# Kernel tuning notes

Hardware: AMD Instinct MI355X
Metric: run time of the kernel (lower is better)

## Reference

```python
import jax, jax.numpy as jnp
import numpy as np

L_IN, L_ENC, B = 1024, 1024, 16
D_IN, D_ENC, D_EMB = 512, 512, 512


def setup_inputs() -> dict:
    key = jax.random.key(0)
    ks = jax.random.split(key, 9)
    s_in = 1.0 / np.sqrt(D_IN)
    s_emb = 1.0 / np.sqrt(D_EMB)
    s_enc = 1.0 / np.sqrt(D_ENC)
    return {
        "in_seq": jax.random.normal(ks[0], (L_IN, B, D_IN), jnp.float32),
        "enc_seq": jax.random.normal(ks[1], (L_ENC, B, D_ENC), jnp.float32),
        "prev_target_seq": jax.random.normal(ks[2], (L_IN, B, D_EMB), jnp.float32),
        # torch Linear weights: (out_features, in_features)
        "W_in2enc": jax.random.normal(ks[3], (D_ENC, D_IN), jnp.float32) * s_in,
        "b_in2enc": jnp.zeros((D_ENC,), jnp.float32),
        "W_lab2enc": jax.random.normal(ks[4], (D_ENC, D_EMB), jnp.float32) * s_emb,
        "b_lab2enc": jnp.zeros((D_ENC,), jnp.float32),
        "W_enc2in": jax.random.normal(ks[5], (D_IN, D_ENC), jnp.float32) * s_enc,
        "b_enc2in": jnp.zeros((D_IN,), jnp.float32),
    }


def reference(in_seq, enc_seq, prev_target_seq,
              W_in2enc, b_in2enc, W_lab2enc, b_lab2enc, W_enc2in, b_enc2in):
    # d_vals: (L_in, B, D_enc) = proj(in_seq) + proj(prev_target_seq)
    in_proj = jnp.einsum('lbi,ei->lbe', in_seq, W_in2enc) + b_in2enc
    tgt_proj = jnp.einsum('lbm,em->lbe', prev_target_seq, W_lab2enc) + b_lab2enc
    d_vals = in_proj + tgt_proj
    # raw attention scores: (L_in, L_enc, B) dot products over D_enc
    scores = jnp.einsum('lbe,mbe->lmb', d_vals, enc_seq)
    # sum-normalization (NOT softmax) over the encoder-length axis
    attn = scores / jnp.sum(scores, axis=1, keepdims=True)
    # weighted sum of encoder states: (L_in, B, D_enc)
    context = jnp.einsum('lmb,mbe->lbe', attn, enc_seq)
    # project back to input dim
    return jnp.einsum('lbe,ie->lbi', context, W_enc2in) + b_enc2in
```

## Files before the change

kernel.cpp:

```cpp
#include <hip/hip_runtime.h>
#include <cstdint>

static constexpr int LDR = 8192;

typedef uint16_t u16;
typedef __attribute__((ext_vector_type(8))) short short8;
typedef __attribute__((ext_vector_type(4))) float f32x4;
struct alignas(8) U16x4 { u16 x, y, z, w; };

__device__ __forceinline__ u16 f2bf(float f) {
    union { float f; unsigned u; } v; v.f = f;
    unsigned r = v.u + 0x7fffu + ((v.u >> 16) & 1u);
    return (u16)(r >> 16);
}

__device__ __forceinline__ short8 cvt8(const float4 a, const float4 b) {
    short8 r;
    r[0]=(short)f2bf(a.x); r[1]=(short)f2bf(a.y); r[2]=(short)f2bf(a.z); r[3]=(short)f2bf(a.w);
    r[4]=(short)f2bf(b.x); r[5]=(short)f2bf(b.y); r[6]=(short)f2bf(b.z); r[7]=(short)f2bf(b.w);
    return r;
}

__device__ __forceinline__ void gl_lds16(const u16* g, unsigned ldsaddr) {
    asm volatile("s_mov_b32 m0, %0\n\t"
                 "global_load_lds_dwordx4 %1, off"
                 :: "s"(__builtin_amdgcn_readfirstlane(ldsaddr)), "v"(g)
                 : "memory");
}

template<int MODE>
__device__ __forceinline__ void gemm_body(
    int bx, int by, int z,
    const u16* __restrict__ A, const u16* __restrict__ Bm,
    const float* __restrict__ b1v, const float* __restrict__ b2v,
    const float* __restrict__ b3v, const float* __restrict__ Sinv,
    u16* __restrict__ Cb, float* __restrict__ Cf)
{
    constexpr int K   = (MODE == 1 || MODE == 5) ? 1024 : 512;
    constexpr int BM  = (MODE == 5 || MODE == 6) ? 64 : 128;
    constexpr int NJ  = (BM == 128) ? 4 : 2;
    constexpr int NIA = BM / 32;
    constexpr int NIB = 4;
    constexpr int ASZ = BM * 128;
    constexpr int BSZ = 128 * 128;
    constexpr int LDA = (MODE == 1 || MODE == 5) ? 1024 : 512;
    constexpr int LDB = (MODE == 1 || MODE == 5) ? 1024 : 512;

    extern __shared__ __align__(16) u16 lds[];

    const int row0 = by * BM;
    const int col0 = bx * 128;
    const int tid  = threadIdx.x;
    const int l    = tid & 63, w = tid >> 6;
    const int wm   = (BM == 128) ? (w >> 1) : 0;
    const int wn   = (BM == 128) ? (w & 1) : w;
    const int quad = l >> 4, l16 = l & 15;

    const u16* Ab = A;
    const u16* Bb = Bm;
    if constexpr (MODE == 5) { Ab = A + z*524288; Bb = Bm + z*524288; }
    if constexpr (MODE == 6) { Bb = Bm + z*262144; }
    if constexpr (MODE == 4) { Ab = A + z*524288; Bb = Bm + z*262144; }

    const int lq = l >> 3;
    const int loffu = ((l & 7) ^ lq) * 8;
    const u16* gA[NIA];
    #pragma unroll
    for (int i = 0; i < NIA; ++i)
        gA[i] = Ab + (size_t)(row0 + i*32 + w*8 + lq) * LDA + loffu;
    const u16* gB[NIB];
    #pragma unroll
    for (int i = 0; i < NIB; ++i)
        gB[i] = Bb + (size_t)(col0 + i*32 + w*8 + lq) * LDB + loffu;

    const unsigned lbase = (unsigned)(size_t)&lds[0];

    auto stage = [&](int c) {
        #pragma unroll
        for (int i = 0; i < NIA; ++i) {
            gl_lds16(gA[i], lbase + c*ASZ + i*4096 + w*1024);
            gA[i] += 64;
        }
        #pragma unroll
        for (int i = 0; i < NIB; ++i) {
            gl_lds16(gB[i], lbase + 2*ASZ + c*BSZ + i*4096 + w*1024);
            gB[i] += 64;
        }
    };

    f32x4 acc[4][NJ] = {};
    const int swzr = (l16 & 7) << 3;
    const int arow = wm * 64;
    const int brow = wn * (BM == 128 ? 64 : 32);

    stage(0);
    int cur = 0;
    for (int kb = 0; kb < K; kb += 64) {
        asm volatile("s_waitcnt vmcnt(0)" ::: "memory");
        __syncthreads();
        if (kb + 64 < K) stage(cur ^ 1);
        const int abase = cur * (ASZ/2);
        const int bbase = ASZ + cur * (BSZ/2);
        #pragma unroll
        for (int kk = 0; kk < 2; ++kk) {
            const int koff = (kk*32 + quad*8) ^ swzr;
            short8 af[4], bfr[NJ];
            #pragma unroll
            for (int i = 0; i < 4; ++i)
                af[i] = *(const short8*)&lds[abase + (arow + i*16 + l16)*64 + koff];
            #pragma unroll
            for (int j = 0; j < NJ; ++j)
                bfr[j] = *(const short8*)&lds[bbase + (brow + j*16 + l16)*64 + koff];
            #pragma unroll
            for (int i = 0; i < 4; ++i)
                #pragma unroll
                for (int j = 0; j < NJ; ++j)
                    acc[i][j] = __builtin_amdgcn_mfma_f32_16x16x32_bf16(af[i], bfr[j], acc[i][j], 0, 0, 0);
        }
        cur ^= 1;
    }

    #pragma unroll
    for (int i = 0; i < 4; ++i) {
        const int grow = row0 + arow + i*16 + quad*4;
        #pragma unroll
        for (int j = 0; j < NJ; ++j) {
            const int gcol = col0 + brow + j*16 + l16;
            #pragma unroll
            for (int r = 0; r < 4; ++r) {
                float v = acc[i][j][r];
                const int R = grow + r;
                if constexpr (MODE == 1) {
                    v += b1v[gcol] + b2v[gcol];
                    Cb[((R & 15)*1024 + (R >> 4))*512 + gcol] = f2bf(v);
                } else if constexpr (MODE == 5 || MODE == 6) {
                    Cb[z*262144 + R*512 + gcol] = f2bf(v);
                } else {
                    const float s = Sinv[R*16 + z];
                    Cf[(R*16 + z)*512 + gcol] = v * s + b3v[gcol];
                }
            }
        }
    }
}

__device__ __forceinline__ void s_xt_body(
    int bid, const float* __restrict__ X, const float* __restrict__ T,
    const double* __restrict__ u, const double* __restrict__ cd,
    float* __restrict__ Sinv, u16* __restrict__ XT)
{
    const int wave = threadIdx.x >> 6, lane = threadIdx.x & 63;
    const int b = bid & 15, g = bid >> 4;
    const int e = lane * 8;
    double u1r[8], u2r[8];
    #pragma unroll
    for (int k = 0; k < 8; ++k) {
        u1r[k] = u[b*512 + e + k];
        u2r[k] = u[8192 + b*512 + e + k];
    }
    const double cb = cd[b];
    #pragma unroll 2
    for (int i = 0; i < 8; ++i) {
        const int j = g*32 + wave*8 + i;
        const int r = j*16 + b;
        float4 x0 = *(const float4*)&X[r*512 + e];
        float4 x1 = *(const float4*)&X[r*512 + e + 4];
        float4 t0 = *(const float4*)&T[r*512 + e];
        float4 t1 = *(const float4*)&T[r*512 + e + 4];
        double a = 0.0;
        a += (double)x0.x*u1r[0] + (double)x0.y*u1r[1] + (double)x0.z*u1r[2] + (double)x0.w*u1r[3];
        a += (double)x1.x*u1r[4] + (double)x1.y*u1r[5] + (double)x1.z*u1r[6] + (double)x1.w*u1r[7];
        a += (double)t0.x*u2r[0] + (double)t0.y*u2r[1] + (double)t0.z*u2r[2] + (double)t0.w*u2r[3];
        a += (double)t1.x*u2r[4] + (double)t1.y*u2r[5] + (double)t1.z*u2r[6] + (double)t1.w*u2r[7];
        *(short8*)&XT[r*1024 + e]       = cvt8(x0, x1);
        *(short8*)&XT[r*1024 + 512 + e] = cvt8(t0, t1);
        #pragma unroll
        for (int off = 32; off > 0; off >>= 1) a += __shfl_down(a, off, 64);
        if (lane == 0) Sinv[r] = (float)(1.0 / (a + cb));
    }
}

__global__ __launch_bounds__(256) void enct_wconv(
    const float* __restrict__ E, u16* __restrict__ EncT, double* __restrict__ part,
    const float* __restrict__ W1, const float* __restrict__ W2,
    const float* __restrict__ W3, u16* __restrict__ W12, u16* __restrict__ W3b)
{
    const int bid = blockIdx.x, t = threadIdx.x;
    if (bid >= 2048) {
        const int idx = (bid - 2048)*256 + t;
        if (idx < 65536) {
            const int r = idx >> 7, k8 = (idx & 127) * 8;
            const float* src = (k8 < 512) ? (W1 + r*512 + k8) : (W2 + r*512 + (k8 - 512));
            float4 a = *(const float4*)src;
            float4 b = *((const float4*)src + 1);
            *(short8*)&W12[r*1024 + k8] = cvt8(a, b);
        } else {
            const int i2 = idx - 65536;
            const int r = i2 >> 6, k8 = (i2 & 63) * 8;
            const float* src = W3 + r*512 + k8;
            float4 a = *(const float4*)src;
            float4 b = *((const float4*)src + 1);
            *(short8*)&W3b[r*512 + k8] = cvt8(a, b);
        }
        return;
    }
    __shared__ float tile[64][65];
    __shared__ double sred[256];
    const int ex = bid & 7;
    const int my = (bid >> 3) & 15;
    const int bb = bid >> 7;
    const int m0 = my * 64;
    const int e0 = ex * 64;
    const int tr = t >> 4;
    const int tc4 = (t & 15) * 4;
    #pragma unroll
    for (int it = 0; it < 4; ++it) {
        const int ml = tr + it*16;
        float4 v = *(const float4*)&E[(m0+ml)*LDR + bb*512 + e0 + tc4];
        *(float4*)&tile[ml][tc4] = v;
    }
    __syncthreads();
    #pragma unroll
    for (int it = 0; it < 4; ++it) {
        const int el = tr + it*16;
        U16x4 o;
        o.x = f2bf(tile[tc4+0][el]);
        o.y = f2bf(tile[tc4+1][el]);
        o.z = f2bf(tile[tc4+2][el]);
        o.w = f2bf(tile[tc4+3][el]);
        *(U16x4*)&EncT[bb*524288 + (e0+el)*1024 + m0 + tc4] = o;
    }
    const int el = t & 63, mq = t >> 6;
    double a = 0.0;
    #pragma unroll
    for (int j = 0; j < 16; ++j) a += (double)tile[mq*16 + j][el];
    sred[t] = a;
    __syncthreads();
    if (t < 64) {
        double s = sred[t] + sred[t+64] + sred[t+128] + sred[t+192];
        part[my*8192 + bb*512 + e0 + t] = s;
    }
}

__global__ __launch_bounds__(256) void prep80(
    const float* __restrict__ W1, const float* __restrict__ W2,
    const float* __restrict__ b1, const float* __restrict__ b2,
    const double* __restrict__ part, double* __restrict__ u, double* __restrict__ cd)
{
    const int blk = blockIdx.x, tid = threadIdx.x;
    __shared__ double es_l[512];
    __shared__ double red[256];
    int b;
    if (blk < 64) b = (blk & 31) >> 1;
    else          b = blk - 64;
    for (int e = tid; e < 512; e += 256) {
        double s = 0.0;
        #pragma unroll
        for (int c = 0; c < 16; ++c) s += part[c*8192 + b*512 + e];
        es_l[e] = s;
    }
    __syncthreads();
    if (blk < 64) {
        const int which = blk >> 5;
        const int t = (blk & 31)*256 + tid;
        const int i = t & 511;
        const float* W = which ? W2 : W1;
        double a = 0.0;
        for (int e = 0; e < 512; ++e) a += (double)W[e*512 + i] * es_l[e];
        u[which*8192 + t] = a;
    } else {
        double a = 0.0;
        for (int e = tid; e < 512; e += 256) a += (double)(b1[e] + b2[e]) * es_l[e];
        red[tid] = a; __syncthreads();
        for (int s = 128; s > 0; s >>= 1) { if (tid < s) red[tid] += red[tid+s]; __syncthreads(); }
        if (tid == 0) cd[b] = red[0];
    }
}

__global__ __launch_bounds__(256) void fused_a(
    const float* __restrict__ X, const float* __restrict__ T,
    const double* __restrict__ u, const double* __restrict__ cd,
    float* __restrict__ Sinv, u16* __restrict__ XT,
    const u16* __restrict__ EncT, u16* __restrict__ Gram)
{
    const int bid = blockIdx.x;
    if (bid < 512) {
        s_xt_body(bid, X, T, u, cd, Sinv, XT);
    } else {
        const int idx = bid - 512;
        gemm_body<5>(idx & 3, (idx >> 2) & 7, idx >> 5,
                     EncT, EncT, nullptr, nullptr, nullptr, nullptr, Gram, nullptr);
    }
}

__global__ __launch_bounds__(256) void fused_b(
    const u16* __restrict__ XT, const u16* __restrict__ W12,
    const float* __restrict__ b1, const float* __restrict__ b2,
    u16* __restrict__ dvals_g,
    const u16* __restrict__ W3b, const u16* __restrict__ Gram,
    u16* __restrict__ HT)
{
    const int bid = blockIdx.x;
    if (bid < 512) {
        gemm_body<1>(bid & 3, bid >> 2, 0,
                     XT, W12, b1, b2, nullptr, nullptr, dvals_g, nullptr);
    } else {
        const int idx = bid - 512;
        gemm_body<6>(idx & 3, (idx >> 2) & 7, idx >> 5,
                     W3b, Gram, nullptr, nullptr, nullptr, nullptr, HT, nullptr);
    }
}

__global__ __launch_bounds__(256) void gemm_m4(
    const u16* __restrict__ dvals_g, const u16* __restrict__ HT,
    const float* __restrict__ b3, const float* __restrict__ Sinv,
    float* __restrict__ out)
{
    gemm_body<4>(blockIdx.x, blockIdx.y, blockIdx.z,
                 dvals_g, HT, nullptr, nullptr, b3, Sinv, nullptr, out);
}

extern "C" void kernel_launch(void* const* d_in, const int* in_sizes, int n_in,
                              void* d_out, int out_size, void* d_ws, size_t ws_size,
                              hipStream_t stream)
{
    const float* X   = (const float*)d_in[0];
    const float* Enc = (const float*)d_in[1];
    const float* T   = (const float*)d_in[2];
    const float* W1  = (const float*)d_in[3];
    const float* b1  = (const float*)d_in[4];
    const float* W2  = (const float*)d_in[5];
    const float* b2  = (const float*)d_in[6];
    const float* W3  = (const float*)d_in[7];
    const float* b3  = (const float*)d_in[8];
    float* out = (float*)d_out;

    char* w = (char*)d_ws;
    u16*    dvals_g  = (u16*)(w);
    u16*    EncT_bf  = (u16*)(w + 16777216);
    u16*    Gram_bf  = (u16*)(w + 33554432);
    u16*    HT_bf    = (u16*)(w + 41943040);
    u16*    W12      = (u16*)(w + 50331648);
    u16*    W3b      = (u16*)(w + 51380224);
    double* part     = (double*)(w + 51904512);
    double* u        = (double*)(w + 52953088);
    double* cd       = (double*)(w + 53084160);
    float*  Sinv     = (float*)(w + 53084288);
    u16*    XTb      = (u16*)d_out;

    dim3 blk(256);
    enct_wconv <<<dim3(2432), blk, 0, stream>>>(Enc, EncT_bf, part, W1, W2, W3, W12, W3b);
    prep80     <<<dim3(80),   blk, 0, stream>>>(W1, W2, b1, b2, part, u, cd);
    fused_a    <<<dim3(1024), blk, 49152, stream>>>(X, T, u, cd, Sinv, XTb, EncT_bf, Gram_bf);
    fused_b    <<<dim3(1024), blk, 65536, stream>>>(XTb, W12, b1, b2, dvals_g, W3b, Gram_bf, HT_bf);
    gemm_m4    <<<dim3(4, 8, 16), blk, 65536, stream>>>(dvals_g, HT_bf, b3, Sinv, out);
}
```

Measured before the change: 241.6 us.

## Regroup kernel fusions across stages, remap blocks for XCD locality, raise MFMA priority

The Gram GEMM (mode 5) now runs together with the prep reduction, and the HT GEMM (mode 6) is interleaved with the S/XT conversion, so work that does not depend on each other shares a launch. The mode 1 and mode 4 GEMMs each get their own launch. Those launches use a block-index swizzle so that consecutive logical tiles land on the same XCD and share L2. Mode 5 and 6 tiles raise wave priority with s_setprio around the MFMA loop so they are favoured over the co-resident memory-bound blocks. The costs are a different dependency schedule and a prep path that reuses the dynamic LDS.

```diff
diff --git a/kernel.cpp b/kernel.cpp
--- a/kernel.cpp
+++ b/kernel.cpp
@@ -45,6 +45,7 @@
     constexpr int BSZ = 128 * 128;
     constexpr int LDA = (MODE == 1 || MODE == 5) ? 1024 : 512;
     constexpr int LDB = (MODE == 1 || MODE == 5) ? 1024 : 512;
+    constexpr bool PRIO = (MODE == 5 || MODE == 6);
 
     extern __shared__ __align__(16) u16 lds[];
 
@@ -101,6 +102,7 @@
         if (kb + 64 < K) stage(cur ^ 1);
         const int abase = cur * (ASZ/2);
         const int bbase = ASZ + cur * (BSZ/2);
+        if constexpr (PRIO) __builtin_amdgcn_s_setprio(1);
         #pragma unroll
         for (int kk = 0; kk < 2; ++kk) {
             const int koff = (kk*32 + quad*8) ^ swzr;
@@ -117,6 +119,7 @@
                 for (int j = 0; j < NJ; ++j)
                     acc[i][j] = __builtin_amdgcn_mfma_f32_16x16x32_bf16(af[i], bfr[j], acc[i][j], 0, 0, 0);
         }
+        if constexpr (PRIO) __builtin_amdgcn_s_setprio(0);
         cur ^= 1;
     }
 
@@ -242,14 +245,22 @@
     }
 }
 
-__global__ __launch_bounds__(256) void prep80(
+__global__ __launch_bounds__(256) void g5_prep(
+    const u16* __restrict__ EncT, u16* __restrict__ Gram,
     const float* __restrict__ W1, const float* __restrict__ W2,
     const float* __restrict__ b1, const float* __restrict__ b2,
     const double* __restrict__ part, double* __restrict__ u, double* __restrict__ cd)
 {
-    const int blk = blockIdx.x, tid = threadIdx.x;
-    __shared__ double es_l[512];
-    __shared__ double red[256];
+    const int bid = blockIdx.x, tid = threadIdx.x;
+    if (bid < 512) {
+        gemm_body<5>(bid & 3, (bid >> 2) & 7, bid >> 5,
+                     EncT, EncT, nullptr, nullptr, nullptr, nullptr, Gram, nullptr);
+        return;
+    }
+    extern __shared__ __align__(16) u16 lds[];
+    double* es_l = (double*)lds;
+    double* red  = (double*)((char*)lds + 4096);
+    const int blk = bid - 512;
     int b;
     if (blk < 64) b = (blk & 31) >> 1;
     else          b = blk - 64;
@@ -277,38 +288,31 @@
     }
 }
 
-__global__ __launch_bounds__(256) void fused_a(
+__global__ __launch_bounds__(256) void g6_sxt(
+    const u16* __restrict__ W3b, const u16* __restrict__ Gram, u16* __restrict__ HT,
     const float* __restrict__ X, const float* __restrict__ T,
     const double* __restrict__ u, const double* __restrict__ cd,
-    float* __restrict__ Sinv, u16* __restrict__ XT,
-    const u16* __restrict__ EncT, u16* __restrict__ Gram)
+    float* __restrict__ Sinv, u16* __restrict__ XT)
 {
     const int bid = blockIdx.x;
-    if (bid < 512) {
-        s_xt_body(bid, X, T, u, cd, Sinv, XT);
+    const int idx = bid >> 1;
+    if (bid & 1) {
+        s_xt_body(idx, X, T, u, cd, Sinv, XT);
     } else {
-        const int idx = bid - 512;
-        gemm_body<5>(idx & 3, (idx >> 2) & 7, idx >> 5,
-                     EncT, EncT, nullptr, nullptr, nullptr, nullptr, Gram, nullptr);
-    }
-}
-
-__global__ __launch_bounds__(256) void fused_b(
+        gemm_body<6>(idx & 3, (idx >> 2) & 7, idx >> 5,
+                     W3b, Gram, nullptr, nullptr, nullptr, nullptr, HT, nullptr);
+    }
+}
+
+__global__ __launch_bounds__(256) void gemm_m1(
     const u16* __restrict__ XT, const u16* __restrict__ W12,
     const float* __restrict__ b1, const float* __restrict__ b2,
-    u16* __restrict__ dvals_g,
-    const u16* __restrict__ W3b, const u16* __restrict__ Gram,
-    u16* __restrict__ HT)
+    u16* __restrict__ dvals_g)
 {
     const int bid = blockIdx.x;
-    if (bid < 512) {
-        gemm_body<1>(bid & 3, bid >> 2, 0,
-                     XT, W12, b1, b2, nullptr, nullptr, dvals_g, nullptr);
-    } else {
-        const int idx = bid - 512;
-        gemm_body<6>(idx & 3, (idx >> 2) & 7, idx >> 5,
-                     W3b, Gram, nullptr, nullptr, nullptr, nullptr, HT, nullptr);
-    }
+    const int logical = (bid & 7)*64 + (bid >> 3);
+    gemm_body<1>(logical & 3, logical >> 2, 0,
+                 XT, W12, b1, b2, nullptr, nullptr, dvals_g, nullptr);
 }
 
 __global__ __launch_bounds__(256) void gemm_m4(
@@ -316,7 +320,9 @@
     const float* __restrict__ b3, const float* __restrict__ Sinv,
     float* __restrict__ out)
 {
-    gemm_body<4>(blockIdx.x, blockIdx.y, blockIdx.z,
+    const int bid = blockIdx.x;
+    const int logical = (bid & 7)*64 + (bid >> 3);
+    gemm_body<4>(logical & 3, (logical >> 2) & 7, logical >> 5,
                  dvals_g, HT, nullptr, nullptr, b3, Sinv, nullptr, out);
 }
 
@@ -349,9 +355,9 @@
     u16*    XTb      = (u16*)d_out;
 
     dim3 blk(256);
-    enct_wconv <<<dim3(2432), blk, 0, stream>>>(Enc, EncT_bf, part, W1, W2, W3, W12, W3b);
-    prep80     <<<dim3(80),   blk, 0, stream>>>(W1, W2, b1, b2, part, u, cd);
-    fused_a    <<<dim3(1024), blk, 49152, stream>>>(X, T, u, cd, Sinv, XTb, EncT_bf, Gram_bf);
-    fused_b    <<<dim3(1024), blk, 65536, stream>>>(XTb, W12, b1, b2, dvals_g, W3b, Gram_bf, HT_bf);
-    gemm_m4    <<<dim3(4, 8, 16), blk, 65536, stream>>>(dvals_g, HT_bf, b3, Sinv, out);
-}
+    enct_wconv <<<dim3(2432), blk, 0,     stream>>>(Enc, EncT_bf, part, W1, W2, W3, W12, W3b);
+    g5_prep    <<<dim3(592),  blk, 49152, stream>>>(EncT_bf, Gram_bf, W1, W2, b1, b2, part, u, cd);
+    g6_sxt     <<<dim3(1024), blk, 49152, stream>>>(W3b, Gram_bf, HT_bf, X, T, u, cd, Sinv, XTb);
+    gemm_m1    <<<dim3(512),  blk, 65536, stream>>>(XTb, W12, b1, b2, dvals_g);
+    gemm_m4    <<<dim3(512),  blk, 65536, stream>>>(dvals_g, HT_bf, b3, Sinv, out);
+}
```

After: 238.0 us. About the same (-1.5%).
